# Performance work log

Hardware: AMD Instinct MI355X
Metric: run time of the kernel (lower is better)

Reference implementation:

```python
import jax, jax.numpy as jnp
import numpy as np

EPS = 1e-3  # kernel epsilon used in Performer generalized kernel
B, H, N, D, M = 1, 8, 1024, 64, 128  # batch, heads, seq, dim_heads, nb_features


def _gaussian_orthogonal_matrix(m, d, seed=0):
    # GaussianOrthogonalRandomMatrix with scaling=0: stacked QR blocks, rows
    # rescaled by chi-distributed norms of gaussian d-vectors.
    rng = np.random.default_rng(seed)
    blocks = []
    for _ in range(m // d):
        g = rng.standard_normal((d, d))
        qmat, _ = np.linalg.qr(g)
        blocks.append(qmat.T)
    proj = np.concatenate(blocks, axis=0)  # [m, d], orthonormal rows per block
    mult = np.linalg.norm(rng.standard_normal((m, d)), axis=1)  # chi norms
    return (mult[:, None] * proj).astype(np.float32)


def setup_inputs() -> dict:
    key = jax.random.key(0)
    kq, kk, kv = jax.random.split(key, 3)
    q = jax.random.normal(kq, (B, H, N, D), dtype=jnp.float32)
    k = jax.random.normal(kk, (B, H, N, D), dtype=jnp.float32)
    v = jax.random.normal(kv, (B, H, N, D), dtype=jnp.float32)
    proj = jnp.asarray(_gaussian_orthogonal_matrix(M, D))
    return {"q": q, "k": k, "v": v, "proj": proj}


def _generalized_kernel(x, proj):
    # kernel_fn(relu)( (x / d**0.25) @ proj^T ) + eps
    normalizer = 1.0 / (x.shape[-1] ** 0.25)
    xp = jnp.einsum('bhnd,md->bhnm', x * normalizer, proj)
    return jax.nn.relu(xp) + EPS


def reference(q, k, v, proj):
    qp = _generalized_kernel(q, proj)  # [B,H,N,M]
    kp = _generalized_kernel(k, proj)  # [B,H,N,M]
    # causal linear attention
    k_cumsum = jnp.cumsum(kp, axis=-2)                              # [B,H,N,M]
    context = jnp.einsum('bhnm,bhne->bhnme', kp, v)                 # [B,H,N,M,D]
    context = jnp.cumsum(context, axis=-3)                          # prefix sums over n
    context = context / k_cumsum[..., None]                         # normalize
    out = jnp.einsum('bhnme,bhnm->bhne', context, qp)               # [B,H,N,D]
    return out
```

## Files before the change

### kernel.cpp

```cpp
#include <hip/hip_runtime.h>

static constexpr int H = 8, N = 1024, D = 64, M = 128, CHUNK = 128, NC = 8;
static constexpr float EPS = 1e-3f;
static constexpr float NORM = 0.35355339059327373f;

typedef __attribute__((ext_vector_type(8))) short short8;
typedef __attribute__((ext_vector_type(4))) float f32x4;

__device__ inline unsigned short f2bf(float x) {
    unsigned u = __float_as_uint(x);
    return (unsigned short)((u + 0x7fffu + ((u >> 16) & 1u)) >> 16);
}
__device__ inline float bf2f(unsigned short u) {
    return __uint_as_float(((unsigned)u) << 16);
}
__device__ inline ushort4 pack4(float4 g) {
    return (ushort4){f2bf(g.x), f2bf(g.y), f2bf(g.z), f2bf(g.w)};
}

__global__ __launch_bounds__(512) void k_projg(const float* __restrict__ q,
                                               const float* __restrict__ k,
                                               const float* __restrict__ proj,
                                               const float* __restrict__ v,
                                               unsigned short* __restrict__ qpb,
                                               unsigned short* __restrict__ kpb,
                                               unsigned short* __restrict__ Gpb,
                                               float* __restrict__ kpart) {
    __shared__ __align__(16) short smem[30208];
    short* projb = smem;
    short* xb = smem + 9216;
    short* obuf = smem + 13824;
    short* kpT = smem + 22528;
    short* vT = smem + 27648;
    const int tid = threadIdx.x;
    const int rblk = blockIdx.x;
    const int h = blockIdx.y;
    const int rowbase = h * N + rblk * 32;
    const int lane = tid & 63, wv = tid >> 6;
    const int rt = wv & 3, mh = wv >> 2;
    const int fr = lane & 15, fq = lane >> 4;

    for (int i4 = tid; i4 < 2048; i4 += 512) {
        int m = i4 >> 4, dq = i4 & 15;
        *(ushort4*)&projb[m * 72 + dq * 4] = pack4(*(const float4*)&proj[i4 * 4]);
    }
    {
        int r = tid >> 4, dq = tid & 15;
        float4 g = *(const float4*)&q[(rowbase + r) * D + dq * 4];
        g.x *= NORM; g.y *= NORM; g.z *= NORM; g.w *= NORM;
        *(ushort4*)&xb[r * 72 + dq * 4] = pack4(g);
        float4 gk = *(const float4*)&k[(rowbase + r) * D + dq * 4];
        gk.x *= NORM; gk.y *= NORM; gk.z *= NORM; gk.w *= NORM;
        *(ushort4*)&xb[(32 + r) * 72 + dq * 4] = pack4(gk);
        int rv = tid & 31, e4 = (tid >> 5) * 4;
        float4 gv = *(const float4*)&v[(rowbase + rv) * D + e4];
        vT[(e4 + 0) * 40 + rv] = (short)f2bf(gv.x);
        vT[(e4 + 1) * 40 + rv] = (short)f2bf(gv.y);
        vT[(e4 + 2) * 40 + rv] = (short)f2bf(gv.z);
        vT[(e4 + 3) * 40 + rv] = (short)f2bf(gv.w);
    }
    __syncthreads();

    f32x4 accp[4];
#pragma unroll
    for (int i = 0; i < 4; i++) accp[i] = (f32x4){0.f, 0.f, 0.f, 0.f};
#pragma unroll
    for (int kt = 0; kt < 2; kt++) {
        short8 a = *(const short8*)&xb[(16 * rt + fr) * 72 + kt * 32 + fq * 8];
#pragma unroll
        for (int i = 0; i < 4; i++) {
            const int mt = mh * 4 + i;
            short8 bb = *(const short8*)&projb[(16 * mt + fr) * 72 + kt * 32 + fq * 8];
            accp[i] = __builtin_amdgcn_mfma_f32_16x16x32_bf16(a, bb, accp[i], 0, 0, 0);
        }
    }
#pragma unroll
    for (int i = 0; i < 4; i++) {
        const int mt = mh * 4 + i;
#pragma unroll
        for (int reg = 0; reg < 4; reg++) {
            const int r = 16 * rt + fq * 4 + reg;
            const int m = 16 * mt + fr;
            unsigned short bv = f2bf(fmaxf(accp[i][reg], 0.f) + EPS);
            obuf[r * 136 + m] = (short)bv;
            if (rt >= 2) kpT[m * 40 + (r - 32)] = (short)bv;
        }
    }
    __syncthreads();

    for (int i = tid; i < 2048; i += 512) {
        int r = i >> 5, cu = i & 31;
        ushort4 val = *(const ushort4*)&obuf[r * 136 + cu * 4];
        unsigned short* g = (r < 32) ? &qpb[(rowbase + r) * M + cu * 4]
                                     : &kpb[(rowbase + r - 32) * M + cu * 4];
        *(ushort4*)g = val;
    }
    const int gb = h * 32 + rblk;
    if (tid < 128) {
        float ks = 0.f;
#pragma unroll 8
        for (int r = 0; r < 32; r++) ks += bf2f((unsigned short)kpT[tid * 40 + r]);
        kpart[gb * M + tid] = ks;
    }
    __syncthreads();

    f32x4 gacc[4];
#pragma unroll
    for (int et = 0; et < 4; et++) gacc[et] = (f32x4){0.f, 0.f, 0.f, 0.f};
    {
        short8 a = *(const short8*)&kpT[(16 * wv + fr) * 40 + fq * 8];
#pragma unroll
        for (int et = 0; et < 4; et++) {
            short8 bb = *(const short8*)&vT[(16 * et + fr) * 40 + fq * 8];
            gacc[et] = __builtin_amdgcn_mfma_f32_16x16x32_bf16(a, bb, gacc[et], 0, 0, 0);
        }
    }
#pragma unroll
    for (int et = 0; et < 4; et++)
#pragma unroll
        for (int reg = 0; reg < 4; reg++) {
            const int m = 16 * wv + fq * 4 + reg;
            obuf[m * 68 + 16 * et + fr] = (short)f2bf(gacc[et][reg]);
        }
    __syncthreads();
    for (int i = tid; i < 2048; i += 512) {
        int m = i >> 4, e4 = (i & 15) * 4;
        *(ushort4*)&Gpb[(gb * M + m) * D + e4] = *(const ushort4*)&obuf[m * 68 + e4];
    }
}

__global__ __launch_bounds__(512) void k_attn(const unsigned short* __restrict__ qpb,
                                              const unsigned short* __restrict__ kpb,
                                              const float* __restrict__ kpart,
                                              const unsigned short* __restrict__ Gpb,
                                              const float* __restrict__ v,
                                              float* __restrict__ out) {
    __shared__ __align__(16) short smem[26112];
    short* bufA = smem;
    short* bufB = smem + 4352;
    short* bufC = smem + 21760;
    const int tid = threadIdx.x;
    const int b = blockIdx.x;
    const int sub = blockIdx.y;
    const int h = b >> 3, c = 7 - (b & 7);
    const int chunkbase = h * N + c * CHUNK;
    const int rowstart = chunkbase + sub * 32;
    const int lane = tid & 63, wv = tid >> 6;
    const int rt = wv & 1, js = wv >> 1;
    const int fr = lane & 15, fq = lane >> 4;

    {
        const unsigned int* src = (const unsigned int*)kpb;
        for (int i = tid; i < 8192; i += 512) {
            int j = i >> 6, mu = i & 63;
            ((unsigned int*)&bufB[j * 136])[mu] = src[(chunkbase + j) * 64 + mu];
        }
        const unsigned int* srcq = (const unsigned int*)qpb;
        for (int i = tid; i < 2048; i += 512) {
            int r = i >> 6, mu = i & 63;
            ((unsigned int*)&bufC[r * 136])[mu] = srcq[(rowstart + r) * 64 + mu];
        }
    }
    __syncthreads();

    if (tid < 128) {
        const int m = tid;
        float z = 0.f;
        const int send = c * 4 + sub;
        for (int s = 0; s < send; s++) z += kpart[(h * 32 + s) * M + m];
#pragma unroll 8
        for (int r = 0; r < 32; r++) {
            z += bf2f((unsigned short)bufB[(sub * 32 + r) * 136 + m]);
            bufA[r * 136 + m] = (short)f2bf(
                bf2f((unsigned short)bufC[r * 136 + m]) * __builtin_amdgcn_rcpf(z));
        }
    }
    float s0r[16];
#pragma unroll
    for (int j = 0; j < 16; j++) s0r[j] = 0.f;
    for (int cp = 0; cp < c; cp++) {
#pragma unroll
        for (int p = 0; p < 4; p++) {
            const short* gsrc =
                (const short*)&Gpb[(h * 32 + cp * 4 + p) * (M * D) + tid * 16];
            short8 g0 = *(const short8*)&gsrc[0];
            short8 g1 = *(const short8*)&gsrc[8];
#pragma unroll
            for (int j = 0; j < 8; j++) {
                s0r[j] += bf2f((unsigned short)g0[j]);
                s0r[8 + j] += bf2f((unsigned short)g1[j]);
            }
        }
    }
    __syncthreads();

    const int jtmax = 2 * sub + 2;
    f32x4 acc1[2];
    acc1[0] = (f32x4){0.f, 0.f, 0.f, 0.f};
    acc1[1] = (f32x4){0.f, 0.f, 0.f, 0.f};
#pragma unroll
    for (int kt = 0; kt < 4; kt++) {
        short8 a = *(const short8*)&bufA[(16 * rt + fr) * 136 + kt * 32 + fq * 8];
#pragma unroll
        for (int jl = 0; jl < 2; jl++) {
            const int jt = 2 * js + jl;
            if (jt < jtmax) {
                short8 bb =
                    *(const short8*)&bufB[(16 * jt + fr) * 136 + kt * 32 + fq * 8];
                acc1[jl] =
                    __builtin_amdgcn_mfma_f32_16x16x32_bf16(a, bb, acc1[jl], 0, 0, 0);
            }
        }
    }
    __syncthreads();
#pragma unroll
    for (int jl = 0; jl < 2; jl++) {
        const int jt = 2 * js + jl;
        if (jt < jtmax) {
            const int j = 16 * jt + fr;
#pragma unroll
            for (int reg = 0; reg < 4; reg++) {
                const int nloc = 16 * rt + fq * 4 + reg;
                float val = (j <= sub * 32 + nloc) ? acc1[jl][reg] : 0.f;
                bufC[nloc * 136 + j] = (short)f2bf(val);
            }
        }
    }

    {
        const int m = tid >> 2;
        const int ebase = (tid & 3) * 16;
#pragma unroll
        for (int j = 0; j < 16; j++)
            bufB[(ebase + j) * 136 + m] = (short)f2bf(s0r[j]);
    }
    __syncthreads();

    f32x4 acc2 = (f32x4){0.f, 0.f, 0.f, 0.f};
#pragma unroll
    for (int kt = 0; kt < 4; kt++) {
        short8 a = *(const short8*)&bufA[(16 * rt + fr) * 136 + kt * 32 + fq * 8];
        short8 bb = *(const short8*)&bufB[(16 * js + fr) * 136 + kt * 32 + fq * 8];
        acc2 = __builtin_amdgcn_mfma_f32_16x16x32_bf16(a, bb, acc2, 0, 0, 0);
    }
    __syncthreads();

    for (int i = tid; i < 2048; i += 512) {
        int j = i >> 4, e4 = (i & 15) * 4;
        float4 g = *(const float4*)&v[(chunkbase + j) * D + e4];
        bufB[(e4 + 0) * 136 + j] = (short)f2bf(g.x);
        bufB[(e4 + 1) * 136 + j] = (short)f2bf(g.y);
        bufB[(e4 + 2) * 136 + j] = (short)f2bf(g.z);
        bufB[(e4 + 3) * 136 + j] = (short)f2bf(g.w);
    }
    __syncthreads();

    const int ktmax = sub + 1;
    for (int kt = 0; kt < ktmax; kt++) {
        short8 a = *(const short8*)&bufC[(16 * rt + fr) * 136 + kt * 32 + fq * 8];
        short8 bb = *(const short8*)&bufB[(16 * js + fr) * 136 + kt * 32 + fq * 8];
        acc2 = __builtin_amdgcn_mfma_f32_16x16x32_bf16(a, bb, acc2, 0, 0, 0);
    }

#pragma unroll
    for (int reg = 0; reg < 4; reg++) {
        out[(rowstart + 16 * rt + fq * 4 + reg) * D + 16 * js + fr] = acc2[reg];
    }
}

extern "C" void kernel_launch(void* const* d_in, const int* in_sizes, int n_in,
                              void* d_out, int out_size, void* d_ws, size_t ws_size,
                              hipStream_t stream) {
    const float* q = (const float*)d_in[0];
    const float* k = (const float*)d_in[1];
    const float* v = (const float*)d_in[2];
    const float* proj = (const float*)d_in[3];
    float* out = (float*)d_out;

    float* ws = (float*)d_ws;
    float* kpart = ws;
    unsigned short* qpb = (unsigned short*)(kpart + H * 32 * M);
    unsigned short* kpb = qpb + H * N * M;
    unsigned short* Gpb = kpb + H * N * M;

    k_projg<<<dim3(32, H), 512, 0, stream>>>(q, k, proj, v, qpb, kpb, Gpb,
                                             kpart);
    k_attn<<<dim3(H * NC, 4), 512, 0, stream>>>(qpb, kpb, kpart, Gpb, v, out);
}
```

Before: 89.80 us.

## Split attention blocks across output dim halves with 256 threads and causal-trimmed loads

k_attn now launches twice as many blocks, each with 256 threads, and each block handles half of the 64 output columns (eh = blockIdx.z). The K-projection and V tiles are loaded only up to the causal row limit, and V is staged into a separate shared region alongside the S0 transpose, which removes two barriers. The aim is more parallelism across CUs and less wasted loading. The cost is that the QK^T score tile and the normalised Q rows are recomputed in both halves, so that work is duplicated.

```diff
diff --git a/kernel.cpp b/kernel.cpp
--- a/kernel.cpp
+++ b/kernel.cpp
@@ -129,7 +129,7 @@
     }
 }
 
-__global__ __launch_bounds__(512) void k_attn(const unsigned short* __restrict__ qpb,
+__global__ __launch_bounds__(256) void k_attn(const unsigned short* __restrict__ qpb,
                                               const unsigned short* __restrict__ kpb,
                                               const float* __restrict__ kpart,
                                               const unsigned short* __restrict__ Gpb,
@@ -139,24 +139,28 @@
     short* bufA = smem;
     short* bufB = smem + 4352;
     short* bufC = smem + 21760;
+    short* s0t = bufB;
+    short* vT = bufB + 8704;
     const int tid = threadIdx.x;
     const int b = blockIdx.x;
     const int sub = blockIdx.y;
+    const int eh = blockIdx.z;
     const int h = b >> 3, c = 7 - (b & 7);
     const int chunkbase = h * N + c * CHUNK;
     const int rowstart = chunkbase + sub * 32;
+    const int jrows = (sub + 1) * 32;
     const int lane = tid & 63, wv = tid >> 6;
     const int rt = wv & 1, js = wv >> 1;
     const int fr = lane & 15, fq = lane >> 4;
 
     {
         const unsigned int* src = (const unsigned int*)kpb;
-        for (int i = tid; i < 8192; i += 512) {
+        for (int i = tid; i < jrows * 64; i += 256) {
             int j = i >> 6, mu = i & 63;
             ((unsigned int*)&bufB[j * 136])[mu] = src[(chunkbase + j) * 64 + mu];
         }
         const unsigned int* srcq = (const unsigned int*)qpb;
-        for (int i = tid; i < 2048; i += 512) {
+        for (int i = tid; i < 2048; i += 256) {
             int r = i >> 6, mu = i & 63;
             ((unsigned int*)&bufC[r * 136])[mu] = srcq[(rowstart + r) * 64 + mu];
         }
@@ -178,32 +182,36 @@
     float s0r[16];
 #pragma unroll
     for (int j = 0; j < 16; j++) s0r[j] = 0.f;
-    for (int cp = 0; cp < c; cp++) {
-#pragma unroll
-        for (int p = 0; p < 4; p++) {
-            const short* gsrc =
-                (const short*)&Gpb[(h * 32 + cp * 4 + p) * (M * D) + tid * 16];
-            short8 g0 = *(const short8*)&gsrc[0];
-            short8 g1 = *(const short8*)&gsrc[8];
-#pragma unroll
-            for (int j = 0; j < 8; j++) {
-                s0r[j] += bf2f((unsigned short)g0[j]);
-                s0r[8 + j] += bf2f((unsigned short)g1[j]);
+    {
+        const int m = tid >> 1;
+        const int ebase = eh * 32 + (tid & 1) * 16;
+        for (int cp = 0; cp < c; cp++) {
+#pragma unroll
+            for (int p = 0; p < 4; p++) {
+                const short* gsrc =
+                    (const short*)&Gpb[((h * 32 + cp * 4 + p) * M + m) * D + ebase];
+                short8 g0 = *(const short8*)&gsrc[0];
+                short8 g1 = *(const short8*)&gsrc[8];
+#pragma unroll
+                for (int j = 0; j < 8; j++) {
+                    s0r[j] += bf2f((unsigned short)g0[j]);
+                    s0r[8 + j] += bf2f((unsigned short)g1[j]);
+                }
             }
         }
     }
     __syncthreads();
 
     const int jtmax = 2 * sub + 2;
-    f32x4 acc1[2];
-    acc1[0] = (f32x4){0.f, 0.f, 0.f, 0.f};
-    acc1[1] = (f32x4){0.f, 0.f, 0.f, 0.f};
+    f32x4 acc1[4];
+#pragma unroll
+    for (int jl = 0; jl < 4; jl++) acc1[jl] = (f32x4){0.f, 0.f, 0.f, 0.f};
 #pragma unroll
     for (int kt = 0; kt < 4; kt++) {
         short8 a = *(const short8*)&bufA[(16 * rt + fr) * 136 + kt * 32 + fq * 8];
 #pragma unroll
-        for (int jl = 0; jl < 2; jl++) {
-            const int jt = 2 * js + jl;
+        for (int jl = 0; jl < 4; jl++) {
+            const int jt = js * 4 + jl;
             if (jt < jtmax) {
                 short8 bb =
                     *(const short8*)&bufB[(16 * jt + fr) * 136 + kt * 32 + fq * 8];
@@ -213,9 +221,10 @@
         }
     }
     __syncthreads();
-#pragma unroll
-    for (int jl = 0; jl < 2; jl++) {
-        const int jt = 2 * js + jl;
+
+#pragma unroll
+    for (int jl = 0; jl < 4; jl++) {
+        const int jt = js * 4 + jl;
         if (jt < jtmax) {
             const int j = 16 * jt + fr;
 #pragma unroll
@@ -226,13 +235,20 @@
             }
         }
     }
-
-    {
-        const int m = tid >> 2;
-        const int ebase = (tid & 3) * 16;
+    {
+        const int m = tid >> 1;
+        const int el = (tid & 1) * 16;
 #pragma unroll
         for (int j = 0; j < 16; j++)
-            bufB[(ebase + j) * 136 + m] = (short)f2bf(s0r[j]);
+            s0t[(el + j) * 136 + m] = (short)f2bf(s0r[j]);
+    }
+    for (int i = tid; i < jrows * 8; i += 256) {
+        int j = i >> 3, e4 = (i & 7) * 4;
+        float4 g = *(const float4*)&v[(chunkbase + j) * D + eh * 32 + e4];
+        vT[(e4 + 0) * 136 + j] = (short)f2bf(g.x);
+        vT[(e4 + 1) * 136 + j] = (short)f2bf(g.y);
+        vT[(e4 + 2) * 136 + j] = (short)f2bf(g.z);
+        vT[(e4 + 3) * 136 + j] = (short)f2bf(g.w);
     }
     __syncthreads();
 
@@ -240,31 +256,20 @@
 #pragma unroll
     for (int kt = 0; kt < 4; kt++) {
         short8 a = *(const short8*)&bufA[(16 * rt + fr) * 136 + kt * 32 + fq * 8];
-        short8 bb = *(const short8*)&bufB[(16 * js + fr) * 136 + kt * 32 + fq * 8];
+        short8 bb = *(const short8*)&s0t[(16 * js + fr) * 136 + kt * 32 + fq * 8];
         acc2 = __builtin_amdgcn_mfma_f32_16x16x32_bf16(a, bb, acc2, 0, 0, 0);
     }
-    __syncthreads();
-
-    for (int i = tid; i < 2048; i += 512) {
-        int j = i >> 4, e4 = (i & 15) * 4;
-        float4 g = *(const float4*)&v[(chunkbase + j) * D + e4];
-        bufB[(e4 + 0) * 136 + j] = (short)f2bf(g.x);
-        bufB[(e4 + 1) * 136 + j] = (short)f2bf(g.y);
-        bufB[(e4 + 2) * 136 + j] = (short)f2bf(g.z);
-        bufB[(e4 + 3) * 136 + j] = (short)f2bf(g.w);
-    }
-    __syncthreads();
-
     const int ktmax = sub + 1;
     for (int kt = 0; kt < ktmax; kt++) {
         short8 a = *(const short8*)&bufC[(16 * rt + fr) * 136 + kt * 32 + fq * 8];
-        short8 bb = *(const short8*)&bufB[(16 * js + fr) * 136 + kt * 32 + fq * 8];
+        short8 bb = *(const short8*)&vT[(16 * js + fr) * 136 + kt * 32 + fq * 8];
         acc2 = __builtin_amdgcn_mfma_f32_16x16x32_bf16(a, bb, acc2, 0, 0, 0);
     }
 
 #pragma unroll
     for (int reg = 0; reg < 4; reg++) {
-        out[(rowstart + 16 * rt + fq * 4 + reg) * D + 16 * js + fr] = acc2[reg];
+        out[(rowstart + 16 * rt + fq * 4 + reg) * D + eh * 32 + 16 * js + fr] =
+            acc2[reg];
     }
 }
 
@@ -285,5 +290,6 @@
 
     k_projg<<<dim3(32, H), 512, 0, stream>>>(q, k, proj, v, qpb, kpb, Gpb,
                                              kpart);
-    k_attn<<<dim3(H * NC, 4), 512, 0, stream>>>(qpb, kpb, kpart, Gpb, v, out);
-}
+    k_attn<<<dim3(H * NC, 4, 2), 256, 0, stream>>>(qpb, kpb, kpart, Gpb, v,
+                                                   out);
+}
```

After: 91.01 us. No clear change (+1.3%).
